# Optimization experiments

Hardware: AMD Instinct MI355X
Metric: run time of the kernel (lower is better)

## Reference

```python
import jax, jax.numpy as jnp
import numpy as np

DIM = 256
HEADS = 8


def setup_inputs() -> dict:
    key = jax.random.key(0)
    ks = jax.random.split(key, 12)
    B, N, L, C, H = 2, 1024, 4096, DIM, HEADS
    s = C ** -0.5
    inp = {
        "query": jax.random.normal(ks[0], (B, N, C), jnp.float32),
        "key": jax.random.normal(ks[1], (B, L, C), jnp.float32),
        "value": jax.random.normal(ks[2], (B, L, C), jnp.float32),
        "key_padding_mask": jnp.zeros((B, L), jnp.bool_),
        "hw_lvl": 1,
        # nn.Linear weights, stored as (out, in) like torch
        "Wq": jax.random.normal(ks[3], (C, C), jnp.float32) * s,
        "Wk": jax.random.normal(ks[4], (C, C), jnp.float32) * s,
        "Wv": jax.random.normal(ks[5], (C, C), jnp.float32) * s,
        "Wp": jax.random.normal(ks[6], (C, C), jnp.float32) * s,
        "bp": jax.random.normal(ks[7], (C,), jnp.float32) * 0.02,
        "W1": jax.random.normal(ks[8], (H, H), jnp.float32) * H ** -0.5,
        "b1": jax.random.normal(ks[9], (H,), jnp.float32) * 0.02,
        "W2": jax.random.normal(ks[10], (1, H), jnp.float32) * H ** -0.5,
        "b2": jax.random.normal(ks[11], (1,), jnp.float32) * 0.02,
    }
    return inp


def reference(query, key, value, key_padding_mask, hw_lvl,
              Wq, Wk, Wv, Wp, bp, W1, b1, W2, b2):
    # key_padding_mask and hw_lvl are accepted but unused by the original module.
    B, N, C = query.shape
    L = key.shape[1]
    H = W1.shape[0]
    D = C // H
    scale = D ** -0.5

    q = (query @ Wq.T).reshape(B, N, H, D)  # bnhd
    k = (key @ Wk.T).reshape(B, L, H, D)    # blhd
    v = (value @ Wv.T).reshape(B, L, H, D)  # blhd

    # raw attention scores [B, H, N, L]
    attn = jnp.einsum("bnhd,blhd->bhnl", q, k) * scale

    # per-score tiny MLP over the head axis -> mask [B, N, L, 1]
    scores_nlh = attn.transpose(0, 2, 3, 1)  # [B, N, L, H]
    new_feats = jax.nn.relu(scores_nlh @ W1.T + b1)
    mask = jax.nn.relu(new_feats @ W2.T + b2)  # [B, N, L, 1]

    a = jax.nn.softmax(attn, axis=-1)  # dropout p=0 -> identity
    x = jnp.einsum("bhnl,blhd->bnhd", a, v).reshape(B, N, C)
    x = x @ Wp.T + bp
    return x, mask
```

## Files before the change

kernel.cpp:

```cpp
#include <hip/hip_runtime.h>

typedef unsigned short u16;
typedef unsigned int u32;
typedef __attribute__((ext_vector_type(8))) short bf16x8;
typedef __attribute__((ext_vector_type(4))) short bf16x4;
typedef __attribute__((ext_vector_type(4))) float f32x4;

#define QK_SCALE 0.17677669529663687f
#define PST 272

__device__ inline float bf2f(u16 h) {
    u32 u = ((u32)h) << 16; float f; __builtin_memcpy(&f, &u, 4); return f;
}
__device__ inline u16 f2bf(float f) {
    u32 u; __builtin_memcpy(&u, &f, 4);
    u = u + 0x7fffu + ((u >> 16) & 1u);
    return (u16)(u >> 16);
}
__device__ inline bf16x8 cvt8(const float* __restrict__ p) {
    bf16x8 o;
#pragma unroll
    for (int i = 0; i < 8; ++i) o[i] = (short)f2bf(p[i]);
    return o;
}

__global__ __launch_bounds__(256) void projf_kernel(
    const float* __restrict__ query, const float* __restrict__ key,
    const float* __restrict__ value,
    const float* __restrict__ Wq, const float* __restrict__ Wk,
    const float* __restrict__ Wv, const float* __restrict__ Wp,
    u16* __restrict__ qb, u16* __restrict__ kb, u16* __restrict__ vt,
    u16* __restrict__ wpb)
{
    const int bx = blockIdx.x;
    const int tid = threadIdx.x;
    if (bx >= 1152) {
        const int idx = (bx - 1152) * 2048 + tid * 8;
        *(bf16x8*)(wpb + idx) = cvt8(Wp + idx);
        return;
    }
    const float *X, *W; u16* outb; int m0, mode;
    if (bx < 128)      { X = query; W = Wq; outb = qb; m0 = bx * 16; mode = 2; }
    else if (bx < 640) { X = key;   W = Wk; outb = kb; m0 = (bx - 128) * 16; mode = 0; }
    else               { X = value; W = Wv; outb = vt; m0 = (bx - 640) * 16; mode = 1; }

    __shared__ __align__(16) u16 xs[16 * PST];
    __shared__ __align__(16) u16 ws[64 * PST];

    {
        const int row = tid >> 4, col = (tid & 15) * 16;
        const float* src = X + (long)(m0 + row) * 256 + col;
        *(bf16x8*)(&xs[row * PST + col])     = cvt8(src);
        *(bf16x8*)(&xs[row * PST + col + 8]) = cvt8(src + 8);
    }

    const int lane = tid & 63, w = tid >> 6;
    const int r = lane & 15, g = lane >> 4;

    for (int by = 0; by < 4; ++by) {
        __syncthreads();
        {
            const int row = tid >> 2, col = (tid & 3) * 64;
            const float* src = W + (long)(by * 64 + row) * 256 + col;
#pragma unroll
            for (int s = 0; s < 4; ++s) {
                *(bf16x8*)(&ws[row * PST + col + s * 16])     = cvt8(src + s * 16);
                *(bf16x8*)(&ws[row * PST + col + s * 16 + 8]) = cvt8(src + s * 16 + 8);
            }
        }
        __syncthreads();

        f32x4 acc = {0.f, 0.f, 0.f, 0.f};
#pragma unroll
        for (int ks = 0; ks < 8; ++ks) {
            bf16x8 a = *(const bf16x8*)(&xs[r * PST + ks * 32 + g * 8]);
            bf16x8 b = *(const bf16x8*)(&ws[(w * 16 + r) * PST + ks * 32 + g * 8]);
            acc = __builtin_amdgcn_mfma_f32_16x16x32_bf16(a, b, acc, 0, 0, 0);
        }

        const int c = by * 64 + w * 16 + r;
        if (mode == 1) {
            const int m_ = m0 + g * 4;
            const int b = m_ >> 12, l = m_ & 4095;
            bf16x4 pk;
#pragma unroll
            for (int j = 0; j < 4; ++j) pk[j] = (short)f2bf(acc[j]);
            *(bf16x4*)(vt + (long)b * 1048576 + (long)(l >> 2) * 1024 + c * 4) = pk;
        } else {
#pragma unroll
            for (int j = 0; j < 4; ++j) {
                const int m = m0 + g * 4 + j;
                if (mode == 2) outb[(long)m * 256 + c] = f2bf(acc[j] * QK_SCALE);
                else           outb[(long)m * 256 + c] = f2bf(acc[j]);
            }
        }
    }
}

__global__ __launch_bounds__(256, 2) void attn_split_kernel(
    const u16* __restrict__ qb, const u16* __restrict__ kb,
    const u16* __restrict__ vt,
    const float* __restrict__ W1, const float* __restrict__ b1,
    const float* __restrict__ W2, const float* __restrict__ b2,
    u16* __restrict__ Opart, float* __restrict__ stats,
    float* __restrict__ out)
{
    __shared__ float ored[4][8][2][2][16][4];
    __shared__ float rs[4][8][16];

    const int tid = threadIdx.x;
    const int w = tid >> 6, lane = tid & 63;
    const int r = lane & 15, g = lane >> 4;
    const int bid = blockIdx.x;
    const int cz = bid & 7;
    const int bi = bid >> 9;
    const int n0 = ((bid >> 3) & 63) * 16;

    float w1r[64], b1r[8], w2r[8];
#pragma unroll
    for (int i = 0; i < 64; ++i) w1r[i] = W1[i];
#pragma unroll
    for (int i = 0; i < 8; ++i) { b1r[i] = b1[i]; w2r[i] = W2[i]; }
    const float b2r = b2[0];

    bf16x8 qh[8];
    const long qbase = (long)(bi * 1024 + n0 + r) * 256 + g * 8;
#pragma unroll
    for (int h = 0; h < 8; ++h)
        qh[h] = *(const bf16x8*)(qb + qbase + h * 32);

    f32x4 oacc[8][2];
#pragma unroll
    for (int h = 0; h < 8; ++h)
#pragma unroll
        for (int c = 0; c < 2; ++c) oacc[h][c] = (f32x4){0.f, 0.f, 0.f, 0.f};
    float rsum[8];
#pragma unroll
    for (int h = 0; h < 8; ++h) rsum[h] = 0.f;

    bf16x8 kf[8];
    {
        const long kbb = (long)(bi * 4096 + cz * 512 + w * 16 + r) * 256 + g * 8;
#pragma unroll
        for (int h = 0; h < 8; ++h)
            kf[h] = *(const bf16x8*)(kb + kbb + h * 32);
    }

    for (int t = 0; t < 8; ++t) {
        const int l0 = cz * 512 + t * 64;

        f32x4 ss[8];
#pragma unroll
        for (int h = 0; h < 8; ++h) {
            f32x4 z = {0.f, 0.f, 0.f, 0.f};
            ss[h] = __builtin_amdgcn_mfma_f32_16x16x32_bf16(kf[h], qh[h], z, 0, 0, 0);
        }

        if (t < 7) {
            const long kbb = (long)(bi * 4096 + l0 + 64 + w * 16 + r) * 256 + g * 8;
#pragma unroll
            for (int h = 0; h < 8; ++h)
                kf[h] = *(const bf16x8*)(kb + kbb + h * 32);
        }

        bf16x4 vf[8][2];
        {
            const u16* vb = vt + (long)bi * 1048576 +
                            (long)((l0 >> 2) + w * 4 + g) * 1024;
#pragma unroll
            for (int h = 0; h < 8; ++h)
#pragma unroll
                for (int c = 0; c < 2; ++c)
                    vf[h][c] = *(const bf16x4*)(vb + (h * 32 + c * 16 + r) * 4);
        }

        {
            f32x4 mv4;
#pragma unroll
            for (int j = 0; j < 4; ++j) {
                float mv = b2r;
#pragma unroll
                for (int f = 0; f < 8; ++f) {
                    float ft = b1r[f];
#pragma unroll
                    for (int h = 0; h < 8; ++h)
                        ft = fmaf(ss[h][j], w1r[f * 8 + h], ft);
                    mv = fmaf(fmaxf(ft, 0.f), w2r[f], mv);
                }
                mv4[j] = fmaxf(mv, 0.f);
            }
            *(f32x4*)(out + 524288l + (long)(bi * 1024 + n0 + r) * 4096
                      + l0 + w * 16 + g * 4) = mv4;
        }

        bf16x4 pa[8];
#pragma unroll
        for (int h = 0; h < 8; ++h) {
            float e0 = __expf(ss[h][0] - 8.f);
            float e1 = __expf(ss[h][1] - 8.f);
            float e2 = __expf(ss[h][2] - 8.f);
            float e3 = __expf(ss[h][3] - 8.f);
            rsum[h] += (e0 + e1) + (e2 + e3);
            u32 u0, u1, u2, u3;
            __builtin_memcpy(&u0, &e0, 4); __builtin_memcpy(&u1, &e1, 4);
            __builtin_memcpy(&u2, &e2, 4); __builtin_memcpy(&u3, &e3, 4);
            u32 lohi[2];
            lohi[0] = (u0 >> 16) | (u1 & 0xFFFF0000u);
            lohi[1] = (u2 >> 16) | (u3 & 0xFFFF0000u);
            __builtin_memcpy(&pa[h], lohi, 8);
        }

#pragma unroll
        for (int h = 0; h < 8; ++h)
#pragma unroll
            for (int c = 0; c < 2; ++c)
                oacc[h][c] = __builtin_amdgcn_mfma_f32_16x16x16bf16_1k(
                    pa[h], vf[h][c], oacc[h][c], 0, 0, 0);
    }

#pragma unroll
    for (int h = 0; h < 8; ++h) {
        float v = rsum[h];
        v += __shfl_xor(v, 16);
        v += __shfl_xor(v, 32);
        if (g == 0) rs[w][h][r] = v;
    }
#pragma unroll
    for (int ph = 0; ph < 2; ++ph) {
        if ((g >> 1) == ph) {
#pragma unroll
            for (int h = 0; h < 8; ++h)
#pragma unroll
                for (int c = 0; c < 2; ++c)
                    *(f32x4*)&ored[w][h][c][g & 1][r][0] = oacc[h][c];
        }
        __syncthreads();
        if (ph == 0 && tid < 128) {
            const int h = tid >> 4, n = tid & 15;
            stats[((long)(bi * 8 + cz) * 8 + h) * 1024 + n0 + n] =
                rs[0][h][n] + rs[1][h][n] + rs[2][h][n] + rs[3][h][n];
        }
        {
            const int h = tid >> 5, c = (tid >> 4) & 1, rr = tid & 15;
#pragma unroll
            for (int g2 = 0; g2 < 2; ++g2)
#pragma unroll
                for (int j = 0; j < 4; ++j) {
                    const float val =
                        ored[0][h][c][g2][rr][j] + ored[1][h][c][g2][rr][j] +
                        ored[2][h][c][g2][rr][j] + ored[3][h][c][g2][rr][j];
                    const int n = (ph * 2 + g2) * 4 + j;
                    Opart[((long)(bi * 8 + cz) * 1024 + n0 + n) * 256
                          + h * 32 + c * 16 + rr] = f2bf(val);
                }
        }
        if (ph == 0) __syncthreads();
    }
}

__global__ __launch_bounds__(512) void reduce_kernel(
    const u16* __restrict__ Opart, const float* __restrict__ stats,
    const u16* __restrict__ wpb, const float* __restrict__ bp,
    float* __restrict__ out)
{
    __shared__ __align__(16) u16 xt[16 * 272];
    const int tid = threadIdx.x;
    const int bi = blockIdx.y, n0 = blockIdx.x * 16, bz = blockIdx.z;

    {
        const int n = tid >> 5, cg = tid & 31, h = cg >> 2;
        float S = 0.f, O[8];
#pragma unroll
        for (int k = 0; k < 8; ++k) O[k] = 0.f;
#pragma unroll
        for (int c = 0; c < 8; ++c) {
            S += stats[((long)(bi * 8 + c) * 8 + h) * 1024 + n0 + n];
            bf16x8 v0 = *(const bf16x8*)(Opart +
                ((long)(bi * 8 + c) * 1024 + n0 + n) * 256 + cg * 8);
#pragma unroll
            for (int k = 0; k < 8; ++k) O[k] += bf2f((u16)v0[k]);
        }
        const float inv = 1.f / S;
        bf16x8 pk;
#pragma unroll
        for (int k = 0; k < 8; ++k) pk[k] = (short)f2bf(O[k] * inv);
        *(bf16x8*)(&xt[n * 272 + cg * 8]) = pk;
    }
    __syncthreads();

    const int w = tid >> 6, lane = tid & 63;
    const int r = lane & 15, g = lane >> 4;
    bf16x8 a8[8];
#pragma unroll
    for (int ks = 0; ks < 8; ++ks)
        a8[ks] = *(const bf16x8*)(&xt[r * 272 + ks * 32 + g * 8]);
    const int cp0 = (bz * 8 + w) * 16;
    f32x4 acc = {0.f, 0.f, 0.f, 0.f};
#pragma unroll
    for (int ks = 0; ks < 8; ++ks) {
        bf16x8 wb = *(const bf16x8*)(wpb + (long)(cp0 + r) * 256 + ks * 32 + g * 8);
        acc = __builtin_amdgcn_mfma_f32_16x16x32_bf16(a8[ks], wb, acc, 0, 0, 0);
    }
    const int cp = cp0 + r;
    const float bpv = bp[cp];
#pragma unroll
    for (int j = 0; j < 4; ++j) {
        const int nn = g * 4 + j;
        out[(long)(bi * 1024 + n0 + nn) * 256 + cp] = acc[j] + bpv;
    }
}

extern "C" void kernel_launch(void* const* d_in, const int* in_sizes, int n_in,
                              void* d_out, int out_size, void* d_ws, size_t ws_size,
                              hipStream_t stream)
{
    const float* query = (const float*)d_in[0];
    const float* key   = (const float*)d_in[1];
    const float* value = (const float*)d_in[2];
    const float* Wq = (const float*)d_in[5];
    const float* Wk = (const float*)d_in[6];
    const float* Wv = (const float*)d_in[7];
    const float* Wp = (const float*)d_in[8];
    const float* bp = (const float*)d_in[9];
    const float* W1 = (const float*)d_in[10];
    const float* b1 = (const float*)d_in[11];
    const float* W2 = (const float*)d_in[12];
    const float* b2 = (const float*)d_in[13];

    u16* qb    = (u16*)d_ws;
    u16* kb    = qb + 524288;
    u16* vtp   = kb + 2097152;
    u16* wpb   = vtp + 2097152;
    u16* Opart = wpb + 65536;
    float* stats = (float*)(Opart + 4194304);
    float* out = (float*)d_out;

    projf_kernel<<<dim3(1184), 256, 0, stream>>>(
        query, key, value, Wq, Wk, Wv, Wp, qb, kb, vtp, wpb);
    attn_split_kernel<<<dim3(1024), 256, 0, stream>>>(
        qb, kb, vtp, W1, b1, W2, b2, Opart, stats, out);
    reduce_kernel<<<dim3(64, 2, 2), 512, 0, stream>>>(Opart, stats, wpb, bp, out);
}
```

Before: 109.2 us.

## Make attention kernel persistent with atomic work queue at three waves per SIMD

Converts the split attention kernel to a persistent grid of 768 blocks that pull work items from a global atomic counter, which is reset by a memset before the launch. To fit three blocks per CU, Q and K fragments are no longer held in registers across the loop; they are reloaded per tile in two halves, and the K prefetch is dropped. The aim is more occupancy and better load balance, at the cost of extra Q reloads, lost K prefetching, and per-item atomics and barriers.

```diff
diff --git a/kernel.cpp b/kernel.cpp
--- a/kernel.cpp
+++ b/kernel.cpp
@@ -97,24 +97,21 @@
     }
 }
 
-__global__ __launch_bounds__(256, 2) void attn_split_kernel(
+__global__ __launch_bounds__(256, 3) void attn_split_kernel(
     const u16* __restrict__ qb, const u16* __restrict__ kb,
     const u16* __restrict__ vt,
     const float* __restrict__ W1, const float* __restrict__ b1,
     const float* __restrict__ W2, const float* __restrict__ b2,
     u16* __restrict__ Opart, float* __restrict__ stats,
-    float* __restrict__ out)
+    u32* __restrict__ ctr, float* __restrict__ out)
 {
     __shared__ float ored[4][8][2][2][16][4];
     __shared__ float rs[4][8][16];
+    __shared__ u32 us;
 
     const int tid = threadIdx.x;
     const int w = tid >> 6, lane = tid & 63;
     const int r = lane & 15, g = lane >> 4;
-    const int bid = blockIdx.x;
-    const int cz = bid & 7;
-    const int bi = bid >> 9;
-    const int n0 = ((bid >> 3) & 63) * 16;
 
     float w1r[64], b1r[8], w2r[8];
 #pragma unroll
@@ -123,138 +120,141 @@
     for (int i = 0; i < 8; ++i) { b1r[i] = b1[i]; w2r[i] = W2[i]; }
     const float b2r = b2[0];
 
-    bf16x8 qh[8];
-    const long qbase = (long)(bi * 1024 + n0 + r) * 256 + g * 8;
-#pragma unroll
-    for (int h = 0; h < 8; ++h)
-        qh[h] = *(const bf16x8*)(qb + qbase + h * 32);
-
-    f32x4 oacc[8][2];
-#pragma unroll
-    for (int h = 0; h < 8; ++h)
-#pragma unroll
-        for (int c = 0; c < 2; ++c) oacc[h][c] = (f32x4){0.f, 0.f, 0.f, 0.f};
-    float rsum[8];
-#pragma unroll
-    for (int h = 0; h < 8; ++h) rsum[h] = 0.f;
-
-    bf16x8 kf[8];
-    {
-        const long kbb = (long)(bi * 4096 + cz * 512 + w * 16 + r) * 256 + g * 8;
+    while (true) {
+        if (tid == 0) us = atomicAdd(ctr, 1u);
+        __syncthreads();
+        const u32 u = us;
+        __syncthreads();
+        if (u >= 1024u) break;
+
+        const int cz = u & 7;
+        const int bi = (int)(u >> 9);
+        const int n0 = ((int)(u >> 3) & 63) * 16;
+
+        f32x4 oacc[8][2];
 #pragma unroll
         for (int h = 0; h < 8; ++h)
-            kf[h] = *(const bf16x8*)(kb + kbb + h * 32);
-    }
-
-    for (int t = 0; t < 8; ++t) {
-        const int l0 = cz * 512 + t * 64;
-
-        f32x4 ss[8];
+#pragma unroll
+            for (int c = 0; c < 2; ++c) oacc[h][c] = (f32x4){0.f, 0.f, 0.f, 0.f};
+        float rsum[8];
+#pragma unroll
+        for (int h = 0; h < 8; ++h) rsum[h] = 0.f;
+
+        for (int t = 0; t < 8; ++t) {
+            const int l0 = cz * 512 + t * 64;
+
+            f32x4 ss[8];
+#pragma unroll
+            for (int hh = 0; hh < 2; ++hh) {
+                bf16x8 qh4[4], kf4[4];
+                const long qa = (long)(bi * 1024 + n0 + r) * 256 + hh * 128 + g * 8;
+                const long ka = (long)(bi * 4096 + l0 + w * 16 + r) * 256 + hh * 128 + g * 8;
+#pragma unroll
+                for (int i = 0; i < 4; ++i) {
+                    qh4[i] = *(const bf16x8*)(qb + qa + i * 32);
+                    kf4[i] = *(const bf16x8*)(kb + ka + i * 32);
+                }
+#pragma unroll
+                for (int i = 0; i < 4; ++i) {
+                    f32x4 z = {0.f, 0.f, 0.f, 0.f};
+                    ss[hh * 4 + i] =
+                        __builtin_amdgcn_mfma_f32_16x16x32_bf16(kf4[i], qh4[i], z, 0, 0, 0);
+                }
+            }
+
+            bf16x4 vf[8][2];
+            {
+                const u16* vb = vt + (long)bi * 1048576 +
+                                (long)((l0 >> 2) + w * 4 + g) * 1024;
+#pragma unroll
+                for (int h = 0; h < 8; ++h)
+#pragma unroll
+                    for (int c = 0; c < 2; ++c)
+                        vf[h][c] = *(const bf16x4*)(vb + (h * 32 + c * 16 + r) * 4);
+            }
+
+            {
+                f32x4 mv4;
+#pragma unroll
+                for (int j = 0; j < 4; ++j) {
+                    float mv = b2r;
+#pragma unroll
+                    for (int f = 0; f < 8; ++f) {
+                        float ft = b1r[f];
+#pragma unroll
+                        for (int h = 0; h < 8; ++h)
+                            ft = fmaf(ss[h][j], w1r[f * 8 + h], ft);
+                        mv = fmaf(fmaxf(ft, 0.f), w2r[f], mv);
+                    }
+                    mv4[j] = fmaxf(mv, 0.f);
+                }
+                *(f32x4*)(out + 524288l + (long)(bi * 1024 + n0 + r) * 4096
+                          + l0 + w * 16 + g * 4) = mv4;
+            }
+
+            bf16x4 pa[8];
+#pragma unroll
+            for (int h = 0; h < 8; ++h) {
+                float e0 = __expf(ss[h][0] - 8.f);
+                float e1 = __expf(ss[h][1] - 8.f);
+                float e2 = __expf(ss[h][2] - 8.f);
+                float e3 = __expf(ss[h][3] - 8.f);
+                rsum[h] += (e0 + e1) + (e2 + e3);
+                u32 u0, u1, u2, u3;
+                __builtin_memcpy(&u0, &e0, 4); __builtin_memcpy(&u1, &e1, 4);
+                __builtin_memcpy(&u2, &e2, 4); __builtin_memcpy(&u3, &e3, 4);
+                u32 lohi[2];
+                lohi[0] = (u0 >> 16) | (u1 & 0xFFFF0000u);
+                lohi[1] = (u2 >> 16) | (u3 & 0xFFFF0000u);
+                __builtin_memcpy(&pa[h], lohi, 8);
+            }
+
+#pragma unroll
+            for (int h = 0; h < 8; ++h)
+#pragma unroll
+                for (int c = 0; c < 2; ++c)
+                    oacc[h][c] = __builtin_amdgcn_mfma_f32_16x16x16bf16_1k(
+                        pa[h], vf[h][c], oacc[h][c], 0, 0, 0);
+        }
+
 #pragma unroll
         for (int h = 0; h < 8; ++h) {
-            f32x4 z = {0.f, 0.f, 0.f, 0.f};
-            ss[h] = __builtin_amdgcn_mfma_f32_16x16x32_bf16(kf[h], qh[h], z, 0, 0, 0);
-        }
-
-        if (t < 7) {
-            const long kbb = (long)(bi * 4096 + l0 + 64 + w * 16 + r) * 256 + g * 8;
-#pragma unroll
-            for (int h = 0; h < 8; ++h)
-                kf[h] = *(const bf16x8*)(kb + kbb + h * 32);
-        }
-
-        bf16x4 vf[8][2];
-        {
-            const u16* vb = vt + (long)bi * 1048576 +
-                            (long)((l0 >> 2) + w * 4 + g) * 1024;
-#pragma unroll
-            for (int h = 0; h < 8; ++h)
-#pragma unroll
-                for (int c = 0; c < 2; ++c)
-                    vf[h][c] = *(const bf16x4*)(vb + (h * 32 + c * 16 + r) * 4);
-        }
-
-        {
-            f32x4 mv4;
-#pragma unroll
-            for (int j = 0; j < 4; ++j) {
-                float mv = b2r;
-#pragma unroll
-                for (int f = 0; f < 8; ++f) {
-                    float ft = b1r[f];
-#pragma unroll
-                    for (int h = 0; h < 8; ++h)
-                        ft = fmaf(ss[h][j], w1r[f * 8 + h], ft);
-                    mv = fmaf(fmaxf(ft, 0.f), w2r[f], mv);
-                }
-                mv4[j] = fmaxf(mv, 0.f);
-            }
-            *(f32x4*)(out + 524288l + (long)(bi * 1024 + n0 + r) * 4096
-                      + l0 + w * 16 + g * 4) = mv4;
-        }
-
-        bf16x4 pa[8];
-#pragma unroll
-        for (int h = 0; h < 8; ++h) {
-            float e0 = __expf(ss[h][0] - 8.f);
-            float e1 = __expf(ss[h][1] - 8.f);
-            float e2 = __expf(ss[h][2] - 8.f);
-            float e3 = __expf(ss[h][3] - 8.f);
-            rsum[h] += (e0 + e1) + (e2 + e3);
-            u32 u0, u1, u2, u3;
-            __builtin_memcpy(&u0, &e0, 4); __builtin_memcpy(&u1, &e1, 4);
-            __builtin_memcpy(&u2, &e2, 4); __builtin_memcpy(&u3, &e3, 4);
-            u32 lohi[2];
-            lohi[0] = (u0 >> 16) | (u1 & 0xFFFF0000u);
-            lohi[1] = (u2 >> 16) | (u3 & 0xFFFF0000u);
-            __builtin_memcpy(&pa[h], lohi, 8);
-        }
-
-#pragma unroll
-        for (int h = 0; h < 8; ++h)
-#pragma unroll
-            for (int c = 0; c < 2; ++c)
-                oacc[h][c] = __builtin_amdgcn_mfma_f32_16x16x16bf16_1k(
-                    pa[h], vf[h][c], oacc[h][c], 0, 0, 0);
-    }
-
-#pragma unroll
-    for (int h = 0; h < 8; ++h) {
-        float v = rsum[h];
-        v += __shfl_xor(v, 16);
-        v += __shfl_xor(v, 32);
-        if (g == 0) rs[w][h][r] = v;
-    }
-#pragma unroll
-    for (int ph = 0; ph < 2; ++ph) {
-        if ((g >> 1) == ph) {
-#pragma unroll
-            for (int h = 0; h < 8; ++h)
-#pragma unroll
-                for (int c = 0; c < 2; ++c)
-                    *(f32x4*)&ored[w][h][c][g & 1][r][0] = oacc[h][c];
-        }
-        __syncthreads();
-        if (ph == 0 && tid < 128) {
-            const int h = tid >> 4, n = tid & 15;
-            stats[((long)(bi * 8 + cz) * 8 + h) * 1024 + n0 + n] =
-                rs[0][h][n] + rs[1][h][n] + rs[2][h][n] + rs[3][h][n];
-        }
-        {
-            const int h = tid >> 5, c = (tid >> 4) & 1, rr = tid & 15;
-#pragma unroll
-            for (int g2 = 0; g2 < 2; ++g2)
-#pragma unroll
-                for (int j = 0; j < 4; ++j) {
-                    const float val =
-                        ored[0][h][c][g2][rr][j] + ored[1][h][c][g2][rr][j] +
-                        ored[2][h][c][g2][rr][j] + ored[3][h][c][g2][rr][j];
-                    const int n = (ph * 2 + g2) * 4 + j;
-                    Opart[((long)(bi * 8 + cz) * 1024 + n0 + n) * 256
-                          + h * 32 + c * 16 + rr] = f2bf(val);
-                }
-        }
-        if (ph == 0) __syncthreads();
+            float v = rsum[h];
+            v += __shfl_xor(v, 16);
+            v += __shfl_xor(v, 32);
+            if (g == 0) rs[w][h][r] = v;
+        }
+#pragma unroll
+        for (int ph = 0; ph < 2; ++ph) {
+            if ((g >> 1) == ph) {
+#pragma unroll
+                for (int h = 0; h < 8; ++h)
+#pragma unroll
+                    for (int c = 0; c < 2; ++c)
+                        *(f32x4*)&ored[w][h][c][g & 1][r][0] = oacc[h][c];
+            }
+            __syncthreads();
+            if (ph == 0 && tid < 128) {
+                const int h = tid >> 4, n = tid & 15;
+                stats[((long)(bi * 8 + cz) * 8 + h) * 1024 + n0 + n] =
+                    rs[0][h][n] + rs[1][h][n] + rs[2][h][n] + rs[3][h][n];
+            }
+            {
+                const int h = tid >> 5, c = (tid >> 4) & 1, rr = tid & 15;
+#pragma unroll
+                for (int g2 = 0; g2 < 2; ++g2)
+#pragma unroll
+                    for (int j = 0; j < 4; ++j) {
+                        const float val =
+                            ored[0][h][c][g2][rr][j] + ored[1][h][c][g2][rr][j] +
+                            ored[2][h][c][g2][rr][j] + ored[3][h][c][g2][rr][j];
+                        const int n = (ph * 2 + g2) * 4 + j;
+                        Opart[((long)(bi * 8 + cz) * 1024 + n0 + n) * 256
+                              + h * 32 + c * 16 + rr] = f2bf(val);
+                    }
+            }
+            __syncthreads();
+        }
     }
 }
 
@@ -333,11 +333,13 @@
     u16* wpb   = vtp + 2097152;
     u16* Opart = wpb + 65536;
     float* stats = (float*)(Opart + 4194304);
+    u32* ctr   = (u32*)(stats + 131072);
     float* out = (float*)d_out;
 
+    hipMemsetAsync(ctr, 0, sizeof(u32), stream);
     projf_kernel<<<dim3(1184), 256, 0, stream>>>(
         query, key, value, Wq, Wk, Wv, Wp, qb, kb, vtp, wpb);
-    attn_split_kernel<<<dim3(1024), 256, 0, stream>>>(
-        qb, kb, vtp, W1, b1, W2, b2, Opart, stats, out);
+    attn_split_kernel<<<dim3(768), 256, 0, stream>>>(
+        qb, kb, vtp, W1, b1, W2, b2, Opart, stats, ctr, out);
     reduce_kernel<<<dim3(64, 2, 2), 512, 0, stream>>>(Opart, stats, wpb, bp, out);
 }
```

Result: slower. 187.9 us (+72.0%).

## Fuse split-L reduction and output projection into attention kernel via arrival counters

Applied to the files above, without the earlier changes.

Removes the separate reduce kernel. Each attention block bumps an atomic counter per (batch, 16-row tile), and the last of the 8 L-split blocks to arrive combines the partials, normalizes by the summed stats and applies the output projection plus bias. This drops one kernel launch and the gap between kernels, at the cost of an extra memset, threadfences and a serialized tail in the last-arriving blocks, which now loop over all 256 output columns with 256 threads.

```diff
diff --git a/kernel.cpp b/kernel.cpp
--- a/kernel.cpp
+++ b/kernel.cpp
@@ -102,11 +102,14 @@
     const u16* __restrict__ vt,
     const float* __restrict__ W1, const float* __restrict__ b1,
     const float* __restrict__ W2, const float* __restrict__ b2,
+    const u16* __restrict__ wpb, const float* __restrict__ bp,
     u16* __restrict__ Opart, float* __restrict__ stats,
-    float* __restrict__ out)
+    u32* __restrict__ done, float* __restrict__ out)
 {
     __shared__ float ored[4][8][2][2][16][4];
     __shared__ float rs[4][8][16];
+    __shared__ __align__(16) u16 xt[16 * 272];
+    __shared__ u32 arrival;
 
     const int tid = threadIdx.x;
     const int w = tid >> 6, lane = tid & 63;
@@ -114,7 +117,8 @@
     const int bid = blockIdx.x;
     const int cz = bid & 7;
     const int bi = bid >> 9;
-    const int n0 = ((bid >> 3) & 63) * 16;
+    const int nidx = (bid >> 3) & 63;
+    const int n0 = nidx * 16;
 
     float w1r[64], b1r[8], w2r[8];
 #pragma unroll
@@ -256,57 +260,58 @@
         }
         if (ph == 0) __syncthreads();
     }
-}
-
-__global__ __launch_bounds__(512) void reduce_kernel(
-    const u16* __restrict__ Opart, const float* __restrict__ stats,
-    const u16* __restrict__ wpb, const float* __restrict__ bp,
-    float* __restrict__ out)
-{
-    __shared__ __align__(16) u16 xt[16 * 272];
-    const int tid = threadIdx.x;
-    const int bi = blockIdx.y, n0 = blockIdx.x * 16, bz = blockIdx.z;
+
+    __threadfence();
+    __syncthreads();
+    if (tid == 0) arrival = atomicAdd(&done[bi * 64 + nidx], 1u);
+    __syncthreads();
+    if (arrival != 7u) return;
+    __threadfence();
 
     {
-        const int n = tid >> 5, cg = tid & 31, h = cg >> 2;
-        float S = 0.f, O[8];
-#pragma unroll
-        for (int k = 0; k < 8; ++k) O[k] = 0.f;
+        const int n = tid >> 4, cg = tid & 15, h = cg >> 1;
+        float S = 0.f, O[16];
+#pragma unroll
+        for (int k = 0; k < 16; ++k) O[k] = 0.f;
 #pragma unroll
         for (int c = 0; c < 8; ++c) {
             S += stats[((long)(bi * 8 + c) * 8 + h) * 1024 + n0 + n];
-            bf16x8 v0 = *(const bf16x8*)(Opart +
-                ((long)(bi * 8 + c) * 1024 + n0 + n) * 256 + cg * 8);
-#pragma unroll
-            for (int k = 0; k < 8; ++k) O[k] += bf2f((u16)v0[k]);
+            const bf16x8* op = (const bf16x8*)(Opart +
+                ((long)(bi * 8 + c) * 1024 + n0 + n) * 256 + cg * 16);
+            bf16x8 v0 = op[0], v1 = op[1];
+#pragma unroll
+            for (int k = 0; k < 8; ++k) {
+                O[k]     += bf2f((u16)v0[k]);
+                O[k + 8] += bf2f((u16)v1[k]);
+            }
         }
         const float inv = 1.f / S;
-        bf16x8 pk;
-#pragma unroll
-        for (int k = 0; k < 8; ++k) pk[k] = (short)f2bf(O[k] * inv);
-        *(bf16x8*)(&xt[n * 272 + cg * 8]) = pk;
+#pragma unroll
+        for (int k = 0; k < 16; ++k)
+            xt[n * 272 + cg * 16 + k] = f2bf(O[k] * inv);
     }
     __syncthreads();
 
-    const int w = tid >> 6, lane = tid & 63;
-    const int r = lane & 15, g = lane >> 4;
     bf16x8 a8[8];
 #pragma unroll
     for (int ks = 0; ks < 8; ++ks)
         a8[ks] = *(const bf16x8*)(&xt[r * 272 + ks * 32 + g * 8]);
-    const int cp0 = (bz * 8 + w) * 16;
-    f32x4 acc = {0.f, 0.f, 0.f, 0.f};
-#pragma unroll
-    for (int ks = 0; ks < 8; ++ks) {
-        bf16x8 wb = *(const bf16x8*)(wpb + (long)(cp0 + r) * 256 + ks * 32 + g * 8);
-        acc = __builtin_amdgcn_mfma_f32_16x16x32_bf16(a8[ks], wb, acc, 0, 0, 0);
-    }
-    const int cp = cp0 + r;
-    const float bpv = bp[cp];
-#pragma unroll
-    for (int j = 0; j < 4; ++j) {
-        const int nn = g * 4 + j;
-        out[(long)(bi * 1024 + n0 + nn) * 256 + cp] = acc[j] + bpv;
+#pragma unroll
+    for (int kblk = 0; kblk < 4; ++kblk) {
+        const int cp0 = (w + kblk * 4) * 16;
+        f32x4 acc = {0.f, 0.f, 0.f, 0.f};
+#pragma unroll
+        for (int ks = 0; ks < 8; ++ks) {
+            bf16x8 wb = *(const bf16x8*)(wpb + (long)(cp0 + r) * 256 + ks * 32 + g * 8);
+            acc = __builtin_amdgcn_mfma_f32_16x16x32_bf16(a8[ks], wb, acc, 0, 0, 0);
+        }
+        const int cp = cp0 + r;
+        const float bpv = bp[cp];
+#pragma unroll
+        for (int j = 0; j < 4; ++j) {
+            const int nn = g * 4 + j;
+            out[(long)(bi * 1024 + n0 + nn) * 256 + cp] = acc[j] + bpv;
+        }
     }
 }
 
@@ -333,11 +338,12 @@
     u16* wpb   = vtp + 2097152;
     u16* Opart = wpb + 65536;
     float* stats = (float*)(Opart + 4194304);
+    u32* done  = (u32*)(stats + 131072);
     float* out = (float*)d_out;
 
+    hipMemsetAsync(done, 0, 128 * sizeof(u32), stream);
     projf_kernel<<<dim3(1184), 256, 0, stream>>>(
         query, key, value, Wq, Wk, Wv, Wp, qb, kb, vtp, wpb);
     attn_split_kernel<<<dim3(1024), 256, 0, stream>>>(
-        qb, kb, vtp, W1, b1, W2, b2, Opart, stats, out);
-    reduce_kernel<<<dim3(64, 2, 2), 512, 0, stream>>>(Opart, stats, wpb, bp, out);
-}
+        qb, kb, vtp, W1, b1, W2, b2, wpb, bp, Opart, stats, done, out);
+}
```

New measurement: 294.4 us. 169% more time.
